# Kernel tuning notes

Hardware: AMD Instinct MI355X
Metric: run time of the kernel (lower is better)

The kernel has to match this reference:

```python
import jax, jax.numpy as jnp
import numpy as np

G, N_NODES, E, H, D, IN_DIM, NS = 1024, 64, 128, 8, 32, 256, 48
EPS = 1e-6

def setup_inputs() -> dict:
    key = jax.random.key(0)
    ks = jax.random.split(key, 10)
    s = 1.0 / np.sqrt(IN_DIM)
    return {
        'h': jax.random.normal(ks[0], (G * N_NODES, IN_DIM), jnp.float32),
        'Wq': jax.random.normal(ks[1], (IN_DIM, H * D), jnp.float32) * s,
        'bq': jax.random.normal(ks[2], (H * D,), jnp.float32) * 0.01,
        'Wk': jax.random.normal(ks[3], (IN_DIM, H * D), jnp.float32) * s,
        'bk': jax.random.normal(ks[4], (H * D,), jnp.float32) * 0.01,
        'Wv': jax.random.normal(ks[5], (IN_DIM, H * D), jnp.float32) * s,
        'bv': jax.random.normal(ks[6], (H * D,), jnp.float32) * 0.01,
        'src': jax.random.randint(ks[7], (E,), 0, N_NODES, jnp.int32),
        'dst': jax.random.randint(ks[8], (E,), 0, N_NODES, jnp.int32),
        'ns': jax.random.randint(ks[9], (E, NS), 0, N_NODES, jnp.int32),
    }

def reference(h, Wq, bq, Wk, bk, Wv, bv, src, dst, ns):
    # per-node projections, reshaped per-graph: [G, n, H, D]
    Q = (h @ Wq + bq).reshape(G, N_NODES, H, D)
    K = (h @ Wk + bk).reshape(G, N_NODES, H, D)
    V = (h @ Wv + bv).reshape(G, N_NODES, H, D)
    # QK[g, s, h, t] = Q[g,s,h] . K[g,t,h], clamped as in torch .clamp(-5, 5)
    QK = jnp.clip(jnp.einsum('gshd,gthd->gsht', Q, K), -5.0, 5.0)  # [G, n, H, n]
    QKs = QK[:, src]  # rows for each edge's source node: [G, E, H, n]
    # numerator: QK[:, src_e, :, dst_e]
    num = jnp.take_along_axis(
        QKs, jnp.broadcast_to(dst[None, :, None, None].astype(jnp.int32), (G, E, H, 1)), axis=3
    )[..., 0]  # [G, E, H]
    # denominator: sum of QK[:, src_e, :, non_siblings(e)]
    den = jnp.take_along_axis(
        QKs, jnp.broadcast_to(ns[None, :, None, :], (G, E, H, NS)), axis=3
    ).sum(-1)  # [G, E, H]
    score = num / (den + EPS)  # [G, E, H]
    # scatter-sum aggregation: wV[g, dst] += V[g, src] * score; z[g, dst] += score
    msg = V[:, src] * score[..., None]  # [G, E, H, D]
    seg = (jnp.arange(G, dtype=jnp.int32)[:, None] * N_NODES + dst[None, :]).reshape(-1)
    wV = jax.ops.segment_sum(msg.reshape(G * E, H, D), seg, num_segments=G * N_NODES)
    z = jax.ops.segment_sum(score.reshape(G * E, H), seg, num_segments=G * N_NODES)
    return wV / (z[..., None] + EPS)  # [G*n, H, D]
```

## Files before the change

### kernel.cpp

```cpp
#include <hip/hip_runtime.h>

#define NG    1024
#define NN    64
#define NE    128
#define NH    8
#define ND    32
#define INDIM 256
#define NS_   48
#define EPS_  1e-6
#define BK    16

#define GBM   128
#define GBN   128
#define GBK   64

#define WS_QKV_FLOATS ((size_t)NG * NH * 3 * NN * ND)
#define WS_ELIST_OFF  (WS_QKV_FLOATS * sizeof(float))
#define WS_CNT_OFF    (WS_ELIST_OFF + (size_t)NN * 64 * sizeof(unsigned short))
#define WS_NEED2      (WS_CNT_OFF + (size_t)NN * sizeof(int))

typedef _Float16 half8_t __attribute__((ext_vector_type(8)));
typedef _Float16 half4_t __attribute__((ext_vector_type(4)));
typedef float    f32x4_t __attribute__((ext_vector_type(4)));

__global__ __launch_bounds__(256, 4) void qkv_gemm_kernel(
    const float* __restrict__ h,
    const float* __restrict__ Wq, const float* __restrict__ bq,
    const float* __restrict__ Wk, const float* __restrict__ bk,
    float* __restrict__ ws)
{
  const int b    = blockIdx.x;
  const int xcd  = b & 7;
  const int slot = b >> 3;
  const int rt   = xcd * 128 + (slot >> 2);
  const int sel  = (slot >> 1) & 1;
  const int ct   = slot & 1;
  const int tid  = threadIdx.x;

  const float* W  = (sel == 0) ? Wq : Wk;
  const float* bs = (sel == 0) ? bq : bk;

  __shared__ float hT[BK][68];
  __shared__ float wT[BK][132];

  const int ty  = tid >> 5;
  const int tx  = tid & 31;
  const int r8  = ty * 8;
  const int ca  = tx * 4;

  float acc[8][4];
  #pragma unroll
  for (int i = 0; i < 8; ++i)
    #pragma unroll
    for (int j = 0; j < 4; ++j) acc[i][j] = 0.f;

  const int ra  = tid >> 2;
  const int kof = (tid & 3) * 4;
  const int kb2 = tid >> 5;
  const int c4  = (tid & 31) * 4;
  const float* hp0 = h + ((size_t)(rt * 64 + ra)) * INDIM + kof;
  const float* wp0 = W + (size_t)kb2 * (NH * ND) + (ct * 128 + c4);

  float4 pa, pb[2];
  pa = *(const float4*)(hp0);
  #pragma unroll
  for (int j = 0; j < 2; ++j)
    pb[j] = *(const float4*)(wp0 + (size_t)(8 * j) * (NH * ND));

  for (int kc = 0; kc < INDIM / BK; ++kc) {
    __syncthreads();
    hT[kof + 0][ra] = pa.x; hT[kof + 1][ra] = pa.y;
    hT[kof + 2][ra] = pa.z; hT[kof + 3][ra] = pa.w;
    #pragma unroll
    for (int j = 0; j < 2; ++j)
      *(float4*)&wT[kb2 + 8 * j][c4] = pb[j];
    __syncthreads();

    if (kc + 1 < INDIM / BK) {
      const int k0n = (kc + 1) * BK;
      pa = *(const float4*)(hp0 + k0n);
      #pragma unroll
      for (int j = 0; j < 2; ++j)
        pb[j] = *(const float4*)(wp0 + (size_t)(k0n + 8 * j) * (NH * ND));
    }

    #pragma unroll
    for (int k = 0; k < BK; ++k) {
      float4 a0 = *(const float4*)&hT[k][r8];
      float4 a1 = *(const float4*)&hT[k][r8 + 4];
      float4 b0 = *(const float4*)&wT[k][ca];
      const float av[8] = {a0.x, a0.y, a0.z, a0.w, a1.x, a1.y, a1.z, a1.w};
      #pragma unroll
      for (int i = 0; i < 8; ++i) {
        acc[i][0] += av[i] * b0.x;
        acc[i][1] += av[i] * b0.y;
        acc[i][2] += av[i] * b0.z;
        acc[i][3] += av[i] * b0.w;
      }
    }
  }

  const int col = ct * 128 + ca;
  const int hda = col >> 5, d0a = col & 31;
  float ba4[4];
  #pragma unroll
  for (int j = 0; j < 4; ++j) ba4[j] = bs[col + j];

  #pragma unroll
  for (int i = 0; i < 8; ++i) {
    const int r = rt * 64 + r8 + i;
    const int g = r >> 6, n = r & 63;
    float* opa = ws + ((((size_t)(g * NH + hda)) * 3 + sel) * NN + n) * ND + d0a;
    *(float4*)opa = make_float4(acc[i][0] + ba4[0], acc[i][1] + ba4[1],
                                acc[i][2] + ba4[2], acc[i][3] + ba4[3]);
  }
}

__device__ __forceinline__ void* swz_pt(void* base, int row, int k) {
  size_t byte = ((size_t)(row * GBK + k)) * 2;
  byte ^= (size_t)((row & 7) << 4);
  return (void*)((char*)base + byte);
}

__global__ __launch_bounds__(256, 2) void v_gemm_mfma(
    const float* __restrict__ h,
    const float* __restrict__ Wv, const float* __restrict__ bv,
    float* __restrict__ ws)
{
  const int b    = blockIdx.x;
  const int xcd  = b & 7;
  const int slot = b >> 3;
  const int rt   = xcd * 64 + (slot >> 1);
  const int ct   = slot & 1;

  __shared__ __align__(16) _Float16 Ahh[GBM * GBK];
  __shared__ __align__(16) _Float16 Ahl[GBM * GBK];
  __shared__ __align__(16) _Float16 Bhh[GBN * GBK];
  __shared__ __align__(16) _Float16 Bhl[GBN * GBK];

  const int tid  = threadIdx.x;
  const int lane = tid & 63;
  const int wvid = tid >> 6;
  const int wm   = wvid >> 1;
  const int wn   = wvid & 1;
  const int lr   = lane & 15;
  const int lg   = lane >> 4;

  f32x4_t acc0[4][4], acc1[4][4];
  #pragma unroll
  for (int i = 0; i < 4; ++i)
    #pragma unroll
    for (int j = 0; j < 4; ++j) {
      acc0[i][j] = (f32x4_t){0.f, 0.f, 0.f, 0.f};
      acc1[i][j] = (f32x4_t){0.f, 0.f, 0.f, 0.f};
    }

  const float* hA  = h + (size_t)rt * GBM * INDIM;
  const int bnn    = tid >> 1;
  const int bkh    = (tid & 1) * 32;
  const int c0     = ct * GBN;
  const float* wB  = Wv + (size_t)bkh * (NH * ND) + (c0 + bnn);

  for (int kc = 0; kc < INDIM / GBK; ++kc) {
    float4 av4[8];
    #pragma unroll
    for (int i = 0; i < 8; ++i) {
      const int idx = i * 256 + tid;
      const int row = idx >> 4, kq = idx & 15;
      av4[i] = *(const float4*)(hA + (size_t)row * INDIM + kc * GBK + kq * 4);
    }
    float wv32[32];
    #pragma unroll
    for (int j = 0; j < 32; ++j)
      wv32[j] = wB[(size_t)(kc * GBK + j) * (NH * ND)];

    if (kc) __syncthreads();

    #pragma unroll
    for (int i = 0; i < 8; ++i) {
      const int idx = i * 256 + tid;
      const int row = idx >> 4, kq = idx & 15;
      half4_t ph, pl;
      ph[0] = (_Float16)av4[i].x; ph[1] = (_Float16)av4[i].y;
      ph[2] = (_Float16)av4[i].z; ph[3] = (_Float16)av4[i].w;
      pl[0] = (_Float16)((av4[i].x - (float)ph[0]) * 2048.f);
      pl[1] = (_Float16)((av4[i].y - (float)ph[1]) * 2048.f);
      pl[2] = (_Float16)((av4[i].z - (float)ph[2]) * 2048.f);
      pl[3] = (_Float16)((av4[i].w - (float)ph[3]) * 2048.f);
      *(half4_t*)swz_pt(Ahh, row, kq * 4) = ph;
      *(half4_t*)swz_pt(Ahl, row, kq * 4) = pl;
    }
    #pragma unroll
    for (int c = 0; c < 4; ++c) {
      half8_t ph, pl;
      #pragma unroll
      for (int j = 0; j < 8; ++j) {
        const float a  = wv32[c * 8 + j];
        const _Float16 x = (_Float16)a;
        ph[j] = x;
        pl[j] = (_Float16)((a - (float)x) * 2048.f);
      }
      *(half8_t*)swz_pt(Bhh, bnn, bkh + c * 8) = ph;
      *(half8_t*)swz_pt(Bhl, bnn, bkh + c * 8) = pl;
    }
    __syncthreads();

    #pragma unroll
    for (int ks = 0; ks < 2; ++ks) {
      const int kb = ks * 32 + lg * 8;
      half8_t bh[4], bl[4];
      #pragma unroll
      for (int j = 0; j < 4; ++j) {
        const int colr = wn * 64 + j * 16 + lr;
        bh[j] = *(const half8_t*)swz_pt(Bhh, colr, kb);
        bl[j] = *(const half8_t*)swz_pt(Bhl, colr, kb);
      }
      #pragma unroll
      for (int i = 0; i < 4; ++i) {
        const int rowr = wm * 64 + i * 16 + lr;
        const half8_t ah = *(const half8_t*)swz_pt(Ahh, rowr, kb);
        const half8_t al = *(const half8_t*)swz_pt(Ahl, rowr, kb);
        #pragma unroll
        for (int j = 0; j < 4; ++j) {
          acc0[i][j] = __builtin_amdgcn_mfma_f32_16x16x32_f16(
              ah, bh[j], acc0[i][j], 0, 0, 0);
          acc1[i][j] = __builtin_amdgcn_mfma_f32_16x16x32_f16(
              ah, bl[j], acc1[i][j], 0, 0, 0);
          acc1[i][j] = __builtin_amdgcn_mfma_f32_16x16x32_f16(
              al, bh[j], acc1[i][j], 0, 0, 0);
        }
      }
    }
  }

  float bj[4];
  #pragma unroll
  for (int j = 0; j < 4; ++j) bj[j] = bv[c0 + wn * 64 + j * 16 + lr];

  #pragma unroll
  for (int i = 0; i < 4; ++i) {
    #pragma unroll
    for (int r = 0; r < 4; ++r) {
      const int R = rt * GBM + wm * 64 + i * 16 + lg * 4 + r;
      const int g = R >> 6, n = R & 63;
      #pragma unroll
      for (int j = 0; j < 4; ++j) {
        const int col = c0 + wn * 64 + j * 16 + lr;
        const int hd = col >> 5, d = col & 31;
        const float val = acc0[i][j][r] + acc1[i][j][r] * (1.0f / 2048.0f)
                          + bj[j];
        ws[((((size_t)(g * NH + hd)) * 3 + 2) * NN + n) * ND + d] = val;
      }
    }
  }
}

__global__ void edge_setup_kernel(const int* __restrict__ dst,
                                  unsigned short* __restrict__ elist,
                                  int* __restrict__ cnt)
{
  const int n = threadIdx.x;
  if (n < NN) {
    int c = 0;
    for (int e = 0; e < NE; ++e) {
      if (dst[e] == n) {
        if (c < 64) elist[n * 64 + c] = (unsigned short)e;
        ++c;
      }
    }
    cnt[n] = (c > 64) ? 64 : c;
  }
}

__global__ __launch_bounds__(256, 5) void attn_kernel(
    const float* __restrict__ ws,
    const int* __restrict__ src, const int* __restrict__ dst,
    const int* __restrict__ ns,
    const unsigned short* __restrict__ elist_g, const int* __restrict__ cnt_g,
    float* __restrict__ out)
{
  const int hd  = blockIdx.x;
  const int g   = blockIdx.y;
  const int tid = threadIdx.x;
  const int ty  = tid >> 4, tx = tid & 15;

  __shared__ union {
    struct { float QT[32][68]; float KT[32][68]; } a;
    float QK[64][65];
  } uQ;
  __shared__ float Vs[64][36];
  __shared__ float  score_s[NE];
  __shared__ int    srcs[NE], dsts[NE];
  __shared__ double z_s[NN];

  const float* base = ws + ((size_t)(g * NH + hd)) * 3 * (NN * ND);
  {
    const int nr = tid >> 3;
    const int d4 = (tid & 7) * 4;
    #pragma unroll
    for (int half = 0; half < 2; ++half) {
      const int n = half * 32 + nr;
      float4 q = *(const float4*)(base + (size_t)n * ND + d4);
      float4 k = *(const float4*)(base + (size_t)(NN * ND) + (size_t)n * ND + d4);
      float4 v = *(const float4*)(base + (size_t)(2 * NN * ND) + (size_t)n * ND + d4);
      uQ.a.QT[d4 + 0][n] = q.x; uQ.a.QT[d4 + 1][n] = q.y;
      uQ.a.QT[d4 + 2][n] = q.z; uQ.a.QT[d4 + 3][n] = q.w;
      uQ.a.KT[d4 + 0][n] = k.x; uQ.a.KT[d4 + 1][n] = k.y;
      uQ.a.KT[d4 + 2][n] = k.z; uQ.a.KT[d4 + 3][n] = k.w;
      *(float4*)&Vs[n][d4] = v;
    }
  }
  __syncthreads();

  {
    const int s0 = ty * 4, t0 = tx * 4;
    float qk[4][4];
    #pragma unroll
    for (int i = 0; i < 4; ++i)
      #pragma unroll
      for (int j = 0; j < 4; ++j) qk[i][j] = 0.f;
    #pragma unroll
    for (int k = 0; k < ND; ++k) {
      float4 qa = *(const float4*)&uQ.a.QT[k][s0];
      float4 kb = *(const float4*)&uQ.a.KT[k][t0];
      qk[0][0] += qa.x * kb.x; qk[0][1] += qa.x * kb.y; qk[0][2] += qa.x * kb.z; qk[0][3] += qa.x * kb.w;
      qk[1][0] += qa.y * kb.x; qk[1][1] += qa.y * kb.y; qk[1][2] += qa.y * kb.z; qk[1][3] += qa.y * kb.w;
      qk[2][0] += qa.z * kb.x; qk[2][1] += qa.z * kb.y; qk[2][2] += qa.z * kb.z; qk[2][3] += qa.z * kb.w;
      qk[3][0] += qa.w * kb.x; qk[3][1] += qa.w * kb.y; qk[3][2] += qa.w * kb.z; qk[3][3] += qa.w * kb.w;
    }
    __syncthreads();
    #pragma unroll
    for (int i = 0; i < 4; ++i)
      #pragma unroll
      for (int j = 0; j < 4; ++j) {
        float v = qk[i][j];
        v = fminf(5.f, fmaxf(-5.f, v));
        uQ.QK[s0 + i][t0 + j] = v;
      }
  }
  __syncthreads();

  if (tid < NE) {
    const int e = tid;
    const int s = src[e], dd = dst[e];
    srcs[e] = s; dsts[e] = dd;
    const float num = uQ.QK[s][dd];
    double den = 0.0;
    const int* np_ = ns + (size_t)e * NS_;
    #pragma unroll
    for (int j = 0; j < NS_; ++j) den += (double)uQ.QK[s][np_[j]];
    score_s[e] = (float)((double)num / (den + (double)EPS_));
  }
  __syncthreads();

  if (tid < NN) {
    const int cn = cnt_g[tid];
    double zz = 0.0;
    for (int c = 0; c < cn; ++c)
      zz += (double)score_s[elist_g[tid * 64 + c]];
    z_s[tid] = zz;
  }
  __syncthreads();

  {
    const int n  = tid >> 2;
    const int d0 = (tid & 3) * 8;
    float wvv[8];
    #pragma unroll
    for (int i = 0; i < 8; ++i) wvv[i] = 0.f;
    const int cn = cnt_g[n];
    for (int c = 0; c < cn; ++c) {
      const int e  = elist_g[n * 64 + c];
      const float sc = score_s[e];
      const int s  = srcs[e];
      float4 v0 = *(const float4*)&Vs[s][d0];
      float4 v1 = *(const float4*)&Vs[s][d0 + 4];
      wvv[0] += sc * v0.x; wvv[1] += sc * v0.y; wvv[2] += sc * v0.z; wvv[3] += sc * v0.w;
      wvv[4] += sc * v1.x; wvv[5] += sc * v1.y; wvv[6] += sc * v1.z; wvv[7] += sc * v1.w;
    }
    const double zz = z_s[n] + (double)EPS_;
    float o[8];
    #pragma unroll
    for (int i = 0; i < 8; ++i) o[i] = (float)((double)wvv[i] / zz);
    float* op = out + (((size_t)(g * NN + n)) * NH + hd) * ND + d0;
    *(float4*)(op)     = make_float4(o[0], o[1], o[2], o[3]);
    *(float4*)(op + 4) = make_float4(o[4], o[5], o[6], o[7]);
  }
}

__global__ __launch_bounds__(256, 4) void raal_fused_kernel(
    const float* __restrict__ h,
    const float* __restrict__ Wq, const float* __restrict__ bq,
    const float* __restrict__ Wk, const float* __restrict__ bk,
    const float* __restrict__ Wv, const float* __restrict__ bv,
    const int*   __restrict__ src, const int* __restrict__ dst,
    const int*   __restrict__ ns,
    float* __restrict__ out)
{
  const int hd  = blockIdx.x;
  const int g   = blockIdx.y;
  const int tid = threadIdx.x;
  const int ty  = tid >> 4, tx = tid & 15;

  __shared__ union {
    struct { float QT[32][64]; float KT[32][64]; } s2;
    float QK[64][64];
  } uQ;
  __shared__ float Vs[64][32];
  __shared__ union {
    struct { float hT[BK][68]; float wT[BK][100]; } s1;
    struct { float score[NE]; int srcs[NE]; int dsts[NE];
             double z[NN]; unsigned short elist[NN][64]; int cnt[NN]; } s3;
  } uA;

  const int r0 = ty * 4;
  const int c4 = tx * 4;
  const int cv = tx * 2;

  float accqk[4][4], accv[4][2];
  #pragma unroll
  for (int i = 0; i < 4; ++i) {
    #pragma unroll
    for (int j = 0; j < 4; ++j) accqk[i][j] = 0.f;
    accv[i][0] = 0.f; accv[i][1] = 0.f;
  }

  const int lr  = tid >> 2;
  const int lk4 = (tid & 3) * 4;
  const int wr  = ty;
  const int wc  = tx * 2;
  const float* hrow = h + ((size_t)(g * NN + lr)) * INDIM + lk4;
  const size_t wcol = (size_t)hd * ND + wc;

  float4 hv; float2 wq2, wk2, wv2;
  {
    hv  = *(const float4*)(hrow);
    const size_t wro = (size_t)wr * (NH * ND) + wcol;
    wq2 = *(const float2*)(Wq + wro);
    wk2 = *(const float2*)(Wk + wro);
    wv2 = *(const float2*)(Wv + wro);
  }

  for (int kc = 0; kc < INDIM / BK; ++kc) {
    __syncthreads();
    uA.s1.hT[lk4 + 0][lr] = hv.x;
    uA.s1.hT[lk4 + 1][lr] = hv.y;
    uA.s1.hT[lk4 + 2][lr] = hv.z;
    uA.s1.hT[lk4 + 3][lr] = hv.w;
    *(float2*)&uA.s1.wT[wr][ 0 + wc] = wq2;
    *(float2*)&uA.s1.wT[wr][32 + wc] = wk2;
    *(float2*)&uA.s1.wT[wr][64 + wc] = wv2;
    __syncthreads();

    if (kc + 1 < INDIM / BK) {
      const int k0n = (kc + 1) * BK;
      hv  = *(const float4*)(hrow + k0n);
      const size_t wro = (size_t)(k0n + wr) * (NH * ND) + wcol;
      wq2 = *(const float2*)(Wq + wro);
      wk2 = *(const float2*)(Wk + wro);
      wv2 = *(const float2*)(Wv + wro);
    }

    #pragma unroll
    for (int k = 0; k < BK; ++k) {
      float4 a  = *(const float4*)&uA.s1.hT[k][r0];
      float4 b  = *(const float4*)&uA.s1.wT[k][c4];
      float2 bv2 = *(const float2*)&uA.s1.wT[k][64 + cv];
      #pragma unroll
      for (int i = 0; i < 4; ++i) {
        const float ai = (i == 0) ? a.x : (i == 1) ? a.y : (i == 2) ? a.z : a.w;
        accqk[i][0] += ai * b.x;
        accqk[i][1] += ai * b.y;
        accqk[i][2] += ai * b.z;
        accqk[i][3] += ai * b.w;
        accv[i][0]  += ai * bv2.x;
        accv[i][1]  += ai * bv2.y;
      }
    }
  }

  {
    if (tx < 8) {
      #pragma unroll
      for (int j = 0; j < 4; ++j) {
        const int c = c4 + j;
        const float b = bq[hd * ND + c];
        #pragma unroll
        for (int i = 0; i < 4; ++i) uQ.s2.QT[c][r0 + i] = accqk[i][j] + b;
      }
    } else {
      #pragma unroll
      for (int j = 0; j < 4; ++j) {
        const int c = c4 - 32 + j;
        const float b = bk[hd * ND + c];
        #pragma unroll
        for (int i = 0; i < 4; ++i) uQ.s2.KT[c][r0 + i] = accqk[i][j] + b;
      }
    }
    const float b0 = bv[hd * ND + cv], b1 = bv[hd * ND + cv + 1];
    #pragma unroll
    for (int i = 0; i < 4; ++i) {
      Vs[r0 + i][cv]     = accv[i][0] + b0;
      Vs[r0 + i][cv + 1] = accv[i][1] + b1;
    }
  }
  __syncthreads();

  {
    const int s0 = ty * 4, t0 = tx * 4;
    float qk[4][4];
    #pragma unroll
    for (int i = 0; i < 4; ++i)
      #pragma unroll
      for (int j = 0; j < 4; ++j) qk[i][j] = 0.f;
    #pragma unroll
    for (int k = 0; k < ND; ++k) {
      float4 qa = *(const float4*)&uQ.s2.QT[k][s0];
      float4 kb = *(const float4*)&uQ.s2.KT[k][t0];
      qk[0][0] += qa.x * kb.x; qk[0][1] += qa.x * kb.y; qk[0][2] += qa.x * kb.z; qk[0][3] += qa.x * kb.w;
      qk[1][0] += qa.y * kb.x; qk[1][1] += qa.y * kb.y; qk[1][2] += qa.y * kb.z; qk[1][3] += qa.y * kb.w;
      qk[2][0] += qa.z * kb.x; qk[2][1] += qa.z * kb.y; qk[2][2] += qa.z * kb.z; qk[2][3] += qa.z * kb.w;
      qk[3][0] += qa.w * kb.x; qk[3][1] += qa.w * kb.y; qk[3][2] += qa.w * kb.z; qk[3][3] += qa.w * kb.w;
    }
    __syncthreads();
    #pragma unroll
    for (int i = 0; i < 4; ++i)
      #pragma unroll
      for (int j = 0; j < 4; ++j) {
        float v = qk[i][j];
        v = fminf(5.f, fmaxf(-5.f, v));
        uQ.QK[s0 + i][t0 + j] = v;
      }
  }
  __syncthreads();

  if (tid < NE) {
    const int e = tid;
    const int s = src[e], dd = dst[e];
    uA.s3.srcs[e] = s; uA.s3.dsts[e] = dd;
    const float num = uQ.QK[s][dd];
    double den = 0.0;
    const int* np_ = ns + (size_t)e * NS_;
    #pragma unroll
    for (int j = 0; j < NS_; ++j) den += (double)uQ.QK[s][np_[j]];
    uA.s3.score[e] = (float)((double)num / (den + (double)EPS_));
  }
  __syncthreads();

  if (tid < NN) {
    int c = 0; double zz = 0.0;
    for (int e = 0; e < NE; ++e) {
      if (uA.s3.dsts[e] == tid) {
        zz += (double)uA.s3.score[e];
        if (c < 64) uA.s3.elist[tid][c] = (unsigned short)e;
        ++c;
      }
    }
    uA.s3.cnt[tid] = (c > 64) ? 64 : c;
    uA.s3.z[tid]   = zz;
  }
  __syncthreads();

  {
    const int n  = tid >> 2;
    const int d0 = (tid & 3) * 8;
    float wvv[8];
    #pragma unroll
    for (int i = 0; i < 8; ++i) wvv[i] = 0.f;
    const int cn = uA.s3.cnt[n];
    for (int c = 0; c < cn; ++c) {
      const int e  = uA.s3.elist[n][c];
      const float sc = uA.s3.score[e];
      const int s  = uA.s3.srcs[e];
      float4 v0 = *(const float4*)&Vs[s][d0];
      float4 v1 = *(const float4*)&Vs[s][d0 + 4];
      wvv[0] += sc * v0.x; wvv[1] += sc * v0.y; wvv[2] += sc * v0.z; wvv[3] += sc * v0.w;
      wvv[4] += sc * v1.x; wvv[5] += sc * v1.y; wvv[6] += sc * v1.z; wvv[7] += sc * v1.w;
    }
    const double zz = uA.s3.z[n] + (double)EPS_;
    float o[8];
    #pragma unroll
    for (int i = 0; i < 8; ++i) o[i] = (float)((double)wvv[i] / zz);
    float* op = out + (((size_t)(g * NN + n)) * NH + hd) * ND + d0;
    *(float4*)(op)     = make_float4(o[0], o[1], o[2], o[3]);
    *(float4*)(op + 4) = make_float4(o[4], o[5], o[6], o[7]);
  }
}

extern "C" void kernel_launch(void* const* d_in, const int* in_sizes, int n_in,
                              void* d_out, int out_size, void* d_ws, size_t ws_size,
                              hipStream_t stream) {
  const float* h   = (const float*)d_in[0];
  const float* Wq  = (const float*)d_in[1];
  const float* bq  = (const float*)d_in[2];
  const float* Wk  = (const float*)d_in[3];
  const float* bk  = (const float*)d_in[4];
  const float* Wv  = (const float*)d_in[5];
  const float* bv  = (const float*)d_in[6];
  const int*   src = (const int*)d_in[7];
  const int*   dst = (const int*)d_in[8];
  const int*   ns  = (const int*)d_in[9];
  float* out = (float*)d_out;

  dim3 b(256, 1, 1);
  if (ws_size >= WS_NEED2) {
    float* ws = (float*)d_ws;
    unsigned short* elist = (unsigned short*)((char*)d_ws + WS_ELIST_OFF);
    int* cnt = (int*)((char*)d_ws + WS_CNT_OFF);

    hipLaunchKernelGGL(qkv_gemm_kernel, dim3(4096, 1, 1), b, 0, stream,
                       h, Wq, bq, Wk, bk, ws);
    hipLaunchKernelGGL(v_gemm_mfma, dim3(1024, 1, 1), b, 0, stream,
                       h, Wv, bv, ws);
    hipLaunchKernelGGL(edge_setup_kernel, dim3(1, 1, 1), dim3(64, 1, 1), 0, stream,
                       dst, elist, cnt);
    hipLaunchKernelGGL(attn_kernel, dim3(NH, NG, 1), b, 0, stream,
                       ws, src, dst, ns, elist, cnt, out);
  } else {
    hipLaunchKernelGGL(raal_fused_kernel, dim3(NH, NG, 1), b, 0, stream,
                       h, Wq, bq, Wk, bk, Wv, bv, src, dst, ns, out);
  }
}
```

Baseline: 492.6 us.

## Use direct global-to-LDS loads in QK GEMM and fold edge setup into V GEMM

The Q/K projection GEMM now stages h and W tiles with global_load_lds DMA straight into shared memory. This replaces the register-staged prefetch and the transposed scalar LDS stores, and the h tile is now stored row-major and read per-row in the inner loop. The tiny edge-list setup kernel becomes one extra block of the V GEMM launch, which removes a kernel launch. The trade-off is that the register double-buffering overlap between loading the next tile and computing the current one is lost. The new h-tile access pattern may also cause LDS bank conflicts.

After: 454.1 us. -7.8%, faster.

```diff
diff --git a/kernel.cpp b/kernel.cpp
--- a/kernel.cpp
+++ b/kernel.cpp
@@ -22,6 +22,12 @@
 typedef _Float16 half8_t __attribute__((ext_vector_type(8)));
 typedef _Float16 half4_t __attribute__((ext_vector_type(4)));
 typedef float    f32x4_t __attribute__((ext_vector_type(4)));
+
+__device__ __forceinline__ void async_ld16(const float* gp, float* lp) {
+  __builtin_amdgcn_global_load_lds(
+      (const __attribute__((address_space(1))) void*)gp,
+      (__attribute__((address_space(3))) void*)lp, 16, 0, 0);
+}
 
 __global__ __launch_bounds__(256, 4) void qkv_gemm_kernel(
     const float* __restrict__ h,
@@ -40,56 +46,46 @@
   const float* W  = (sel == 0) ? Wq : Wk;
   const float* bs = (sel == 0) ? bq : bk;
 
-  __shared__ float hT[BK][68];
-  __shared__ float wT[BK][132];
+  __shared__ __align__(16) float hT[64][16];
+  __shared__ __align__(16) float wT[16][128];
 
   const int ty  = tid >> 5;
   const int tx  = tid & 31;
   const int r8  = ty * 8;
   const int ca  = tx * 4;
 
+  const int wvid = tid >> 6;
+  const int lane = tid & 63;
+
   float acc[8][4];
   #pragma unroll
   for (int i = 0; i < 8; ++i)
     #pragma unroll
     for (int j = 0; j < 4; ++j) acc[i][j] = 0.f;
 
-  const int ra  = tid >> 2;
-  const int kof = (tid & 3) * 4;
-  const int kb2 = tid >> 5;
-  const int c4  = (tid & 31) * 4;
-  const float* hp0 = h + ((size_t)(rt * 64 + ra)) * INDIM + kof;
-  const float* wp0 = W + (size_t)kb2 * (NH * ND) + (ct * 128 + c4);
-
-  float4 pa, pb[2];
-  pa = *(const float4*)(hp0);
-  #pragma unroll
-  for (int j = 0; j < 2; ++j)
-    pb[j] = *(const float4*)(wp0 + (size_t)(8 * j) * (NH * ND));
+  const float* gA = h + ((size_t)(rt * 64 + wvid * 16 + (lane >> 2))) * INDIM
+                      + (lane & 3) * 4;
+  const float* gB0 = W + ((size_t)(wvid * 4 + 0 + (lane >> 5))) * (NH * ND)
+                       + ct * 128 + (lane & 31) * 4;
+  const float* gB1 = W + ((size_t)(wvid * 4 + 2 + (lane >> 5))) * (NH * ND)
+                       + ct * 128 + (lane & 31) * 4;
+  float* lA  = &hT[wvid * 16][0];
+  float* lB0 = &wT[wvid * 4 + 0][0];
+  float* lB1 = &wT[wvid * 4 + 2][0];
 
   for (int kc = 0; kc < INDIM / BK; ++kc) {
     __syncthreads();
-    hT[kof + 0][ra] = pa.x; hT[kof + 1][ra] = pa.y;
-    hT[kof + 2][ra] = pa.z; hT[kof + 3][ra] = pa.w;
-    #pragma unroll
-    for (int j = 0; j < 2; ++j)
-      *(float4*)&wT[kb2 + 8 * j][c4] = pb[j];
+    async_ld16(gA + kc * 16, lA);
+    async_ld16(gB0 + (size_t)(kc * 16) * (NH * ND), lB0);
+    async_ld16(gB1 + (size_t)(kc * 16) * (NH * ND), lB1);
     __syncthreads();
 
-    if (kc + 1 < INDIM / BK) {
-      const int k0n = (kc + 1) * BK;
-      pa = *(const float4*)(hp0 + k0n);
-      #pragma unroll
-      for (int j = 0; j < 2; ++j)
-        pb[j] = *(const float4*)(wp0 + (size_t)(k0n + 8 * j) * (NH * ND));
-    }
-
     #pragma unroll
     for (int k = 0; k < BK; ++k) {
-      float4 a0 = *(const float4*)&hT[k][r8];
-      float4 a1 = *(const float4*)&hT[k][r8 + 4];
       float4 b0 = *(const float4*)&wT[k][ca];
-      const float av[8] = {a0.x, a0.y, a0.z, a0.w, a1.x, a1.y, a1.z, a1.w};
+      float av[8];
+      #pragma unroll
+      for (int i = 0; i < 8; ++i) av[i] = hT[r8 + i][k];
       #pragma unroll
       for (int i = 0; i < 8; ++i) {
         acc[i][0] += av[i] * b0.x;
@@ -125,9 +121,26 @@
 __global__ __launch_bounds__(256, 2) void v_gemm_mfma(
     const float* __restrict__ h,
     const float* __restrict__ Wv, const float* __restrict__ bv,
+    const int* __restrict__ dst,
+    unsigned short* __restrict__ elist, int* __restrict__ cnt,
     float* __restrict__ ws)
 {
-  const int b    = blockIdx.x;
+  const int b = blockIdx.x;
+  if (b >= 1024) {
+    const int n = threadIdx.x;
+    if (n < NN) {
+      int c = 0;
+      for (int e = 0; e < NE; ++e) {
+        if (dst[e] == n) {
+          if (c < 64) elist[n * 64 + c] = (unsigned short)e;
+          ++c;
+        }
+      }
+      cnt[n] = (c > 64) ? 64 : c;
+    }
+    return;
+  }
+
   const int xcd  = b & 7;
   const int slot = b >> 3;
   const int rt   = xcd * 64 + (slot >> 1);
@@ -252,23 +265,6 @@
         ws[((((size_t)(g * NH + hd)) * 3 + 2) * NN + n) * ND + d] = val;
       }
     }
-  }
-}
-
-__global__ void edge_setup_kernel(const int* __restrict__ dst,
-                                  unsigned short* __restrict__ elist,
-                                  int* __restrict__ cnt)
-{
-  const int n = threadIdx.x;
-  if (n < NN) {
-    int c = 0;
-    for (int e = 0; e < NE; ++e) {
-      if (dst[e] == n) {
-        if (c < 64) elist[n * 64 + c] = (unsigned short)e;
-        ++c;
-      }
-    }
-    cnt[n] = (c > 64) ? 64 : c;
   }
 }
 
@@ -610,10 +606,8 @@
 
     hipLaunchKernelGGL(qkv_gemm_kernel, dim3(4096, 1, 1), b, 0, stream,
                        h, Wq, bq, Wk, bk, ws);
-    hipLaunchKernelGGL(v_gemm_mfma, dim3(1024, 1, 1), b, 0, stream,
-                       h, Wv, bv, ws);
-    hipLaunchKernelGGL(edge_setup_kernel, dim3(1, 1, 1), dim3(64, 1, 1), 0, stream,
-                       dst, elist, cnt);
+    hipLaunchKernelGGL(v_gemm_mfma, dim3(1025, 1, 1), b, 0, stream,
+                       h, Wv, bv, dst, elist, cnt, ws);
     hipLaunchKernelGGL(attn_kernel, dim3(NH, NG, 1), b, 0, stream,
                        ws, src, dst, ns, elist, cnt, out);
   } else {
```
